# Kernel optimization log

Measured on AMD Instinct MI355X. Metric: run time of the kernel, lower is better.

Reference implementation:

```python
import jax, jax.numpy as jnp
import numpy as np

B, S, D, H, L = 4, 2048, 256, 4, 2
DK = D // H
V, T = 32000, 1000


def setup_inputs() -> dict:
    key = jax.random.key(0)
    ks = jax.random.split(key, 20)
    sc = 0.02
    event_emb = jax.random.normal(ks[0], (V, D), jnp.float32) * sc
    event_emb = event_emb.at[0].set(0.0)  # padding_idx=0
    time_emb = jax.random.normal(ks[1], (T, D), jnp.float32) * sc
    inp = {
        "x": jax.random.randint(ks[2], (B, S), 0, V, jnp.int32),
        "time_deltas": jax.random.randint(ks[3], (B, S), 0, T, jnp.int32),
        "mask": jax.random.randint(ks[4], (B, S), 0, 2, jnp.int32),
        "event_emb": event_emb,
        "time_emb": time_emb,
        "Wq": jax.random.normal(ks[5], (L, D, D), jnp.float32) * sc,
        "bq": jnp.zeros((L, D), jnp.float32),
        "Wk": jax.random.normal(ks[6], (L, D, D), jnp.float32) * sc,
        "bk": jnp.zeros((L, D), jnp.float32),
        "Wv": jax.random.normal(ks[7], (L, D, D), jnp.float32) * sc,
        "bv": jnp.zeros((L, D), jnp.float32),
        "time_proj": jax.random.normal(ks[8], (L, T, H), jnp.float32) * sc,
        "Wo": jax.random.normal(ks[9], (L, D, D), jnp.float32) * sc,
        "bo": jnp.zeros((L, D), jnp.float32),
        "ln_g": jnp.ones((L, D), jnp.float32),
        "ln_b": jnp.zeros((L, D), jnp.float32),
        "Wc1": jax.random.normal(ks[10], (D, D // 2), jnp.float32) * sc,
        "bc1": jnp.zeros((D // 2,), jnp.float32),
        "Wc2": jax.random.normal(ks[11], (D // 2, 1), jnp.float32) * sc,
        "bc2": jnp.zeros((1,), jnp.float32),
    }
    return inp


def _layernorm(h, g, b, eps=1e-5):
    mu = jnp.mean(h, -1, keepdims=True)
    var = jnp.mean(jnp.square(h - mu), -1, keepdims=True)
    return (h - mu) * jax.lax.rsqrt(var + eps) * g + b


def _attn(h, t_bins, mask, Wq, bq, Wk, bk, Wv, bv, tp, Wo, bo):
    b, s, d = h.shape
    q = (h @ Wq + bq).reshape(b, s, H, DK)
    k = (h @ Wk + bk).reshape(b, s, H, DK)
    v = (h @ Wv + bv).reshape(b, s, H, DK)
    scores = jnp.einsum("bqhd,bkhd->bhqk", q, k) / np.sqrt(DK).astype(np.float32)
    time_bias = tp[t_bins]  # [b,s,H] -> bias per key position
    scores = scores + jnp.transpose(time_bias, (0, 2, 1))[:, :, None, :]
    scores = jnp.where(mask[:, None, None, :] == 0, -1e9, scores)
    attn = jax.nn.softmax(scores, axis=-1)
    ctx = jnp.einsum("bhqk,bkhd->bqhd", attn, v).reshape(b, s, d)
    return ctx @ Wo + bo


def reference(x, time_deltas, mask, event_emb, time_emb, Wq, bq, Wk, bk, Wv, bv,
              time_proj, Wo, bo, ln_g, ln_b, Wc1, bc1, Wc2, bc2):
    t_bins = jnp.clip(time_deltas, 0, T - 1)
    h = event_emb[x] + time_emb[t_bins]
    for l in range(L):
        h = _attn(h, t_bins, mask, Wq[l], bq[l], Wk[l], bk[l], Wv[l], bv[l],
                  time_proj[l], Wo[l], bo[l])
        h = _layernorm(h, ln_g[l], ln_b[l])
    last = h[:, -1, :]
    hid = jax.nn.relu(last @ Wc1 + bc1)
    return jax.nn.sigmoid(hid @ Wc2 + bc2)
```

## Files before the change

kernel.cpp:

```cpp
#include <hip/hip_runtime.h>
#include <math.h>

namespace {

constexpr int NB = 4, NS = 2048, ND = 256, NH = 4, NDK = 64, NL = 2, NT = 1000;
constexpr float L2E = 1.44269504089f;
constexpr float QSCALE = 0.125f * L2E;

typedef short bfx8 __attribute__((ext_vector_type(8)));
typedef float f32x4 __attribute__((ext_vector_type(4)));
typedef float f32x16 __attribute__((ext_vector_type(16)));

static __device__ __forceinline__ short f2bf(float f) {
  union { float f; unsigned u; } v; v.f = f;
  unsigned u = v.u;
  unsigned r = (u + 0x7fffu + ((u >> 16) & 1u)) >> 16;
  return (short)r;
}
static __device__ __forceinline__ float bf2f(short s) {
  union { float f; unsigned u; } v; v.u = ((unsigned)(unsigned short)s) << 16;
  return v.f;
}
static __device__ __forceinline__ float exp2_hw(float x) {
  float r;
  asm("v_exp_f32 %0, %1" : "=v"(r) : "v"(x));
  return r;
}
static __device__ __forceinline__ unsigned cvt_pk_bf16(float lo, float hi) {
  unsigned d;
  asm("v_cvt_pk_bf16_f32 %0, %1, %2" : "=v"(d) : "v"(lo), "v"(hi));
  return d;
}

__global__ __launch_bounds__(256) void k_packem(const int* __restrict__ x,
                                                const int* __restrict__ td,
                                                const float* __restrict__ ee,
                                                const float* __restrict__ te,
                                                short* __restrict__ hb,
                                                const float* __restrict__ Wq,
                                                const float* __restrict__ Wk,
                                                const float* __restrict__ Wv,
                                                const float* __restrict__ Wo,
                                                const float* __restrict__ bq,
                                                const float* __restrict__ bk,
                                                const float* __restrict__ bv,
                                                short* __restrict__ wqkvT,
                                                short* __restrict__ woT,
                                                float* __restrict__ bqkv) {
  if (blockIdx.x < 128) {
    __shared__ float t[64][65];
    int bi = blockIdx.x;
    int z = bi >> 4, l = z >> 2, mat = z & 3;
    const float* src;
    short* dst;
    float scale = 1.f;
    if (mat == 0)      { src = Wq + (size_t)l * 65536; dst = wqkvT + (size_t)l * 768 * 256; scale = QSCALE; }
    else if (mat == 1) { src = Wk + (size_t)l * 65536; dst = wqkvT + (size_t)l * 768 * 256 + 256 * 256; }
    else if (mat == 2) { src = Wv + (size_t)l * 65536; dst = wqkvT + (size_t)l * 768 * 256 + 512 * 256; }
    else               { src = Wo + (size_t)l * 65536; dst = woT + (size_t)l * 65536; }
    int k0 = (bi & 3) * 64, n0 = ((bi >> 2) & 3) * 64;
    int c = threadIdx.x & 63, r4 = threadIdx.x >> 6;
    #pragma unroll
    for (int rr = 0; rr < 64; rr += 4) t[rr + r4][c] = src[(size_t)(k0 + rr + r4) * 256 + n0 + c];
    __syncthreads();
    #pragma unroll
    for (int rr = 0; rr < 64; rr += 4) {
      int n = rr + r4;
      dst[(size_t)(n0 + n) * 256 + k0 + c] = f2bf(t[c][n] * scale);
    }
    if (mat == 0 && (bi & 15) == 0) {
      for (int cc = threadIdx.x; cc < 768; cc += 256) {
        float v = cc < 256 ? bq[l * 256 + cc] * QSCALE
                           : (cc < 512 ? bk[l * 256 + cc - 256] : bv[l * 256 + cc - 512]);
        bqkv[l * 768 + cc] = v;
      }
    }
  } else {
    int lane = threadIdx.x & 63, r4 = threadIdx.x >> 6;
    int row = (blockIdx.x - 128) * 4 + r4;
    int xi = x[row];
    int tb = td[row];
    tb = tb < 0 ? 0 : (tb >= NT ? NT - 1 : tb);
    float4 e = ((const float4*)&ee[(size_t)xi * ND])[lane];
    float4 tv = ((const float4*)&te[(size_t)tb * ND])[lane];
    short4 ob;
    ob.x = f2bf(e.x + tv.x); ob.y = f2bf(e.y + tv.y);
    ob.z = f2bf(e.z + tv.z); ob.w = f2bf(e.w + tv.w);
    ((short4*)&hb[(size_t)row * ND])[lane] = ob;
  }
}

template <int OUT_BF16>
__global__ __launch_bounds__(256) void k_gemm(const short* __restrict__ A,
                                              const short* __restrict__ BT,
                                              const float* __restrict__ bias,
                                              void* __restrict__ C, int ldc,
                                              int mb_mul, int mb_add, int n_base) {
  constexpr int LP = 76;
  __shared__ short at[64][LP];
  __shared__ short bt[128][LP];
  int tid = threadIdx.x;
  int w = tid >> 6, lane = tid & 63, ln15 = lane & 15, g = lane >> 4;
  int m0 = (blockIdx.x * mb_mul + mb_add) * 64;
  int n0 = n_base + blockIdx.y * 128;
  int srow = tid >> 2, scol = (tid & 3) * 16;
  int brow = tid >> 1, bcol = (tid & 1) * 32;

  f32x4 acc[8];
  #pragma unroll
  for (int nt = 0; nt < 8; ++nt) acc[nt] = (f32x4){0.f, 0.f, 0.f, 0.f};

  bfx8 a0, a1, b0, b1, b2, b3;
  auto LOAD = [&](int kk0) {
    const short* as = &A[(size_t)(m0 + srow) * 256 + kk0 + scol];
    a0 = *(const bfx8*)as; a1 = *(const bfx8*)(as + 8);
    const short* bs = &BT[(size_t)(n0 + brow) * 256 + kk0 + bcol];
    b0 = *(const bfx8*)bs; b1 = *(const bfx8*)(bs + 8);
    b2 = *(const bfx8*)(bs + 16); b3 = *(const bfx8*)(bs + 24);
  };
  LOAD(0);
  for (int kk0 = 0; kk0 < 256; kk0 += 64) {
    __syncthreads();
    *(bfx8*)&at[srow][scol] = a0; *(bfx8*)&at[srow][scol + 8] = a1;
    *(bfx8*)&bt[brow][bcol] = b0; *(bfx8*)&bt[brow][bcol + 8] = b1;
    *(bfx8*)&bt[brow][bcol + 16] = b2; *(bfx8*)&bt[brow][bcol + 24] = b3;
    __syncthreads();
    if (kk0 + 64 < 256) LOAD(kk0 + 64);
    #pragma unroll
    for (int ks = 0; ks < 2; ++ks) {
      bfx8 af = *(const bfx8*)&at[w * 16 + ln15][ks * 32 + g * 8];
      #pragma unroll
      for (int nt = 0; nt < 8; ++nt) {
        bfx8 bf = *(const bfx8*)&bt[nt * 16 + ln15][ks * 32 + g * 8];
        acc[nt] = __builtin_amdgcn_mfma_f32_16x16x32_bf16(af, bf, acc[nt], 0, 0, 0);
      }
    }
  }

  #pragma unroll
  for (int nt = 0; nt < 8; ++nt) {
    int col = n0 + nt * 16 + ln15;
    float bb = bias[col];
    #pragma unroll
    for (int r = 0; r < 4; ++r) {
      int row = m0 + w * 16 + g * 4 + r;
      float val = acc[nt][r] + bb;
      if (OUT_BF16) ((short*)C)[(size_t)row * ldc + col] = f2bf(val);
      else          ((float*)C)[(size_t)row * ldc + col] = val;
    }
  }
}

__global__ __launch_bounds__(256) void k_pmerge(const short* __restrict__ partO,
                                                const float* __restrict__ partML,
                                                const short* __restrict__ BT,
                                                const float* __restrict__ bias,
                                                short* __restrict__ C) {
  constexpr int LP = 76;
  constexpr int NC = 2;
  __shared__ short at[64][LP];
  __shared__ short bt[128][LP];
  int tid = threadIdx.x;
  int w = tid >> 6, lane = tid & 63, ln15 = lane & 15, g = lane >> 4;
  int m0 = blockIdx.x * 64;
  int n0 = blockIdx.y * 128;
  int srow = tid >> 2, scol = (tid & 3) * 16;
  int brow = tid >> 1, bcol = (tid & 1) * 32;

  int grow = m0 + srow;
  int b = grow >> 11, s = grow & 2047;

  f32x4 acc[8];
  #pragma unroll
  for (int nt = 0; nt < 8; ++nt) acc[nt] = (f32x4){0.f, 0.f, 0.f, 0.f};

  bfx8 a0, a1, b0_, b1_, b2_, b3_;
  auto LOAD = [&](int kk0) {
    int hh2 = kk0 >> 6;
    size_t rbase = (size_t)(b * NH + hh2) * NS + s;
    float2 ml[NC];
    float M = -1e30f;
    #pragma unroll
    for (int c = 0; c < NC; ++c) {
      ml[c] = *(const float2*)&partML[(rbase + (size_t)c * 16 * NS) * 2];
      M = fmaxf(M, ml[c].x);
    }
    float wgt[NC], L = 0.f;
    #pragma unroll
    for (int c = 0; c < NC; ++c) { wgt[c] = exp2_hw(ml[c].x - M); L += ml[c].y * wgt[c]; }
    float inv = 1.f / L;
    float av[16];
    #pragma unroll
    for (int i = 0; i < 16; ++i) av[i] = 0.f;
    #pragma unroll
    for (int c = 0; c < NC; ++c) {
      float wc = wgt[c] * inv;
      size_t row = rbase + (size_t)c * 16 * NS;
      union { int4 v; short sh[8]; } ua, ub;
      ua.v = *(const int4*)&partO[row * 64 + scol];
      ub.v = *(const int4*)&partO[row * 64 + scol + 8];
      #pragma unroll
      for (int i = 0; i < 8; ++i) {
        av[i]     = fmaf(bf2f(ua.sh[i]), wc, av[i]);
        av[8 + i] = fmaf(bf2f(ub.sh[i]), wc, av[8 + i]);
      }
    }
    union { bfx8 v; short sh[8]; } pa, pb;
    #pragma unroll
    for (int i = 0; i < 8; ++i) { pa.sh[i] = f2bf(av[i]); pb.sh[i] = f2bf(av[8 + i]); }
    a0 = pa.v; a1 = pb.v;
    const short* bs = &BT[(size_t)(n0 + brow) * 256 + kk0 + bcol];
    b0_ = *(const bfx8*)bs; b1_ = *(const bfx8*)(bs + 8);
    b2_ = *(const bfx8*)(bs + 16); b3_ = *(const bfx8*)(bs + 24);
  };
  LOAD(0);
  for (int kk0 = 0; kk0 < 256; kk0 += 64) {
    __syncthreads();
    *(bfx8*)&at[srow][scol] = a0; *(bfx8*)&at[srow][scol + 8] = a1;
    *(bfx8*)&bt[brow][bcol] = b0_; *(bfx8*)&bt[brow][bcol + 8] = b1_;
    *(bfx8*)&bt[brow][bcol + 16] = b2_; *(bfx8*)&bt[brow][bcol + 24] = b3_;
    __syncthreads();
    if (kk0 + 64 < 256) LOAD(kk0 + 64);
    #pragma unroll
    for (int ks = 0; ks < 2; ++ks) {
      bfx8 af = *(const bfx8*)&at[w * 16 + ln15][ks * 32 + g * 8];
      #pragma unroll
      for (int nt = 0; nt < 8; ++nt) {
        bfx8 bf = *(const bfx8*)&bt[nt * 16 + ln15][ks * 32 + g * 8];
        acc[nt] = __builtin_amdgcn_mfma_f32_16x16x32_bf16(af, bf, acc[nt], 0, 0, 0);
      }
    }
  }

  #pragma unroll
  for (int nt = 0; nt < 8; ++nt) {
    int col = n0 + nt * 16 + ln15;
    float bb = bias[col];
    #pragma unroll
    for (int r = 0; r < 4; ++r) {
      int row = m0 + w * 16 + g * 4 + r;
      C[(size_t)row * 256 + col] = f2bf(acc[nt][r] + bb);
    }
  }
}

__global__ __launch_bounds__(256) void k_gmerge(const short* __restrict__ partO,
                                                const float* __restrict__ partML,
                                                const short* __restrict__ BT,
                                                const float* __restrict__ bias,
                                                float* __restrict__ C) {
  constexpr int LP = 76;
  constexpr int NC = 16;
  __shared__ short at[64][LP];
  __shared__ short bt[128][LP];
  int tid = threadIdx.x;
  int w = tid >> 6, lane = tid & 63, ln15 = lane & 15, g = lane >> 4;
  int m0 = (blockIdx.x * 32 + 31) * 64;
  int n0 = blockIdx.y * 128;
  int srow = tid >> 2, scol = (tid & 3) * 16;
  int brow = tid >> 1, bcol = (tid & 1) * 32;

  int grow = m0 + srow;
  int b = grow >> 11, s = grow & 2047;
  int qloc = s - (NS - 128);

  f32x4 acc[8];
  #pragma unroll
  for (int nt = 0; nt < 8; ++nt) acc[nt] = (f32x4){0.f, 0.f, 0.f, 0.f};

  bfx8 a0, a1, b0_, b1_, b2_, b3_;
  auto LOAD = [&](int kk0) {
    int hh2 = kk0 >> 6;
    size_t rbase = (size_t)(b * NH + hh2) * 128 + qloc;
    float M = -1e30f;
    float mls[NC], lls[NC];
    #pragma unroll
    for (int c = 0; c < NC; ++c) {
      float2 ml = *(const float2*)&partML[(rbase + (size_t)c * 16 * 128) * 2];
      mls[c] = ml.x; lls[c] = ml.y;
      M = fmaxf(M, ml.x);
    }
    float L = 0.f, wgt[NC];
    #pragma unroll
    for (int c = 0; c < NC; ++c) { wgt[c] = exp2_hw(mls[c] - M); L += lls[c] * wgt[c]; }
    float inv = 1.f / L;
    float av[16];
    #pragma unroll
    for (int i = 0; i < 16; ++i) av[i] = 0.f;
    #pragma unroll
    for (int c = 0; c < NC; ++c) {
      float wc = wgt[c] * inv;
      size_t row = rbase + (size_t)c * 16 * 128;
      union { int4 v; short sh[8]; } ua, ub;
      ua.v = *(const int4*)&partO[row * 64 + scol];
      ub.v = *(const int4*)&partO[row * 64 + scol + 8];
      #pragma unroll
      for (int i = 0; i < 8; ++i) {
        av[i]     = fmaf(bf2f(ua.sh[i]), wc, av[i]);
        av[8 + i] = fmaf(bf2f(ub.sh[i]), wc, av[8 + i]);
      }
    }
    union { bfx8 v; short sh[8]; } pa, pb;
    #pragma unroll
    for (int i = 0; i < 8; ++i) { pa.sh[i] = f2bf(av[i]); pb.sh[i] = f2bf(av[8 + i]); }
    a0 = pa.v; a1 = pb.v;
    const short* bs = &BT[(size_t)(n0 + brow) * 256 + kk0 + bcol];
    b0_ = *(const bfx8*)bs; b1_ = *(const bfx8*)(bs + 8);
    b2_ = *(const bfx8*)(bs + 16); b3_ = *(const bfx8*)(bs + 24);
  };
  LOAD(0);
  for (int kk0 = 0; kk0 < 256; kk0 += 64) {
    __syncthreads();
    *(bfx8*)&at[srow][scol] = a0; *(bfx8*)&at[srow][scol + 8] = a1;
    *(bfx8*)&bt[brow][bcol] = b0_; *(bfx8*)&bt[brow][bcol + 8] = b1_;
    *(bfx8*)&bt[brow][bcol + 16] = b2_; *(bfx8*)&bt[brow][bcol + 24] = b3_;
    __syncthreads();
    if (kk0 + 64 < 256) LOAD(kk0 + 64);
    #pragma unroll
    for (int ks = 0; ks < 2; ++ks) {
      bfx8 af = *(const bfx8*)&at[w * 16 + ln15][ks * 32 + g * 8];
      #pragma unroll
      for (int nt = 0; nt < 8; ++nt) {
        bfx8 bf = *(const bfx8*)&bt[nt * 16 + ln15][ks * 32 + g * 8];
        acc[nt] = __builtin_amdgcn_mfma_f32_16x16x32_bf16(af, bf, acc[nt], 0, 0, 0);
      }
    }
  }

  #pragma unroll
  for (int nt = 0; nt < 8; ++nt) {
    int col = n0 + nt * 16 + ln15;
    float bb = bias[col];
    #pragma unroll
    for (int r = 0; r < 4; ++r) {
      int row = m0 + w * 16 + g * 4 + r;
      C[(size_t)row * 256 + col] = acc[nt][r] + bb;
    }
  }
}

__global__ __launch_bounds__(256) void k_frag(const short* __restrict__ qkv,
                                              const int* __restrict__ td,
                                              const int* __restrict__ mask,
                                              const float* __restrict__ tp,
                                              short* __restrict__ vT,
                                              float* __restrict__ sbias_g) {
  __shared__ short vl[64][72];
  int tile = blockIdx.x, hh = blockIdx.y, b = blockIdx.z;
  int t = threadIdx.x;
  int k0 = tile * 64;
  {
    int key = t >> 2, dg = (t & 3) * 16;
    const short* vsrc = &qkv[(size_t)(b * NS + k0 + key) * 768 + 512 + hh * NDK + dg];
    bfx8 v0 = *(const bfx8*)vsrc, v1 = *(const bfx8*)(vsrc + 8);
    *(bfx8*)&vl[key][dg] = v0;
    *(bfx8*)&vl[key][dg + 8] = v1;
  }
  if (t < 64) {
    int kk = k0 + t;
    int tb = td[b * NS + kk];
    tb = tb < 0 ? 0 : (tb >= NT ? NT - 1 : tb);
    sbias_g[(size_t)(b * NH + hh) * NS + kk] = mask[b * NS + kk] ? tp[tb * NH + hh] * L2E : -1e9f;
  }
  __syncthreads();
  int dim = t >> 2, c0 = (t & 3) * 16;
  short outv[16];
  #pragma unroll
  for (int j = 0; j < 16; ++j) outv[j] = vl[c0 + j][dim];
  short* dst = &vT[(((size_t)(b * NH + hh) * 32 + tile) * 64 + dim) * 64 + c0];
  *(int4*)dst = *(const int4*)outv;
  *(int4*)(dst + 8) = *(const int4*)(outv + 8);
}

__global__ __launch_bounds__(256) void k_attn(const short* __restrict__ qkv,
                                              const short* __restrict__ vT,
                                              const float* __restrict__ sbias_g,
                                              short* __restrict__ partO,
                                              float* __restrict__ partML,
                                              int q_base, int qcount, int nchunk) {
  constexpr int LP = 76;
  __shared__ short kt[64][LP];
  __shared__ short vt[64][LP];
  __shared__ float sbias[64];

  int tid = threadIdx.x;
  int w = tid >> 6, lane = tid & 63, q31 = lane & 31, hl = lane >> 5;
  int b = blockIdx.z, hh = blockIdx.y;
  int bh = b * NH + hh;
  int qtile = blockIdx.x / nchunk;
  int chunk = blockIdx.x - qtile * nchunk;
  int niter = NS / (64 * nchunk);
  int tbase = chunk * niter;
  int q0 = q_base + qtile * 128;
  int qq = q0 + w * 32 + q31;

  bfx8 aq[4];
  #pragma unroll
  for (int ki = 0; ki < 4; ++ki)
    aq[ki] = *(const bfx8*)&qkv[(size_t)(b * NS + qq) * 768 + hh * NDK + ki * 16 + hl * 8];

  f32x16 o[2];
  #pragma unroll
  for (int dt = 0; dt < 2; ++dt)
    #pragma unroll
    for (int i = 0; i < 16; ++i) o[dt][i] = 0.f;
  float m = -1e30f, lsum = 0.f;

  int srow = tid >> 2, scg = (tid & 3) * 16;

  bfx8 kr0, kr1, vr0, vr1;
  float br = 0.f;
  auto loadset = [&](int it) {
    int tt = tbase + it;
    int k0 = tt * 64;
    const short* ksrc = &qkv[(size_t)(b * NS + k0 + srow) * 768 + 256 + hh * NDK + scg];
    kr0 = *(const bfx8*)ksrc; kr1 = *(const bfx8*)(ksrc + 8);
    const short* vsrc = &vT[(((size_t)bh * 32 + tt) * 64 + srow) * 64 + scg];
    vr0 = *(const bfx8*)vsrc; vr1 = *(const bfx8*)(vsrc + 8);
    if (tid < 64) br = sbias_g[(size_t)bh * NS + k0 + tid];
  };

  loadset(0);
  for (int it = 0; it < niter; ++it) {
    __syncthreads();
    *(bfx8*)&kt[srow][scg] = kr0;
    *(bfx8*)&kt[srow][scg + 8] = kr1;
    *(bfx8*)&vt[srow][scg] = vr0;
    *(bfx8*)&vt[srow][scg + 8] = vr1;
    if (tid < 64) sbias[tid] = br;
    __syncthreads();
    if (it + 1 < niter) loadset(it + 1);

    f32x16 c[2];
    #pragma unroll
    for (int kt2 = 0; kt2 < 2; ++kt2)
      #pragma unroll
      for (int i = 0; i < 16; ++i) c[kt2][i] = 0.f;
    __builtin_amdgcn_s_setprio(1);
    #pragma unroll
    for (int kt2 = 0; kt2 < 2; ++kt2) {
      #pragma unroll
      for (int ki = 0; ki < 4; ++ki) {
        bfx8 kf = *(const bfx8*)&kt[kt2 * 32 + q31][ki * 16 + hl * 8];
        c[kt2] = __builtin_amdgcn_mfma_f32_32x32x16_bf16(kf, aq[ki], c[kt2], 0, 0, 0);
      }
    }
    __builtin_amdgcn_s_setprio(0);

    #pragma unroll
    for (int kt2 = 0; kt2 < 2; ++kt2) {
      #pragma unroll
      for (int rg = 0; rg < 4; ++rg) {
        float4 bb = *(const float4*)&sbias[kt2 * 32 + rg * 8 + hl * 4];
        c[kt2][rg * 4 + 0] += bb.x; c[kt2][rg * 4 + 1] += bb.y;
        c[kt2][rg * 4 + 2] += bb.z; c[kt2][rg * 4 + 3] += bb.w;
      }
    }
    float rm = c[0][0];
    #pragma unroll
    for (int kt2 = 0; kt2 < 2; ++kt2)
      #pragma unroll
      for (int i = 0; i < 16; ++i) rm = fmaxf(rm, c[kt2][i]);
    rm = fmaxf(rm, __shfl_xor(rm, 32, 64));
    if (__any(rm > m + 10.f)) {
      float nm = fmaxf(m, rm);
      float scl = exp2_hw(m - nm);
      m = nm;
      lsum *= scl;
      #pragma unroll
      for (int dt = 0; dt < 2; ++dt)
        #pragma unroll
        for (int i = 0; i < 16; ++i) o[dt][i] *= scl;
    }
    float ts = 0.f;
    #pragma unroll
    for (int kt2 = 0; kt2 < 2; ++kt2)
      #pragma unroll
      for (int i = 0; i < 16; ++i) { c[kt2][i] = exp2_hw(c[kt2][i] - m); ts += c[kt2][i]; }
    lsum += ts;

    __builtin_amdgcn_s_setprio(1);
    #pragma unroll
    for (int kt2 = 0; kt2 < 2; ++kt2) {
      #pragma unroll
      for (int ks = 0; ks < 2; ++ks) {
        unsigned pa0 = cvt_pk_bf16(c[kt2][8 * ks + 0], c[kt2][8 * ks + 1]);
        unsigned pa1 = cvt_pk_bf16(c[kt2][8 * ks + 2], c[kt2][8 * ks + 3]);
        unsigned pb0 = cvt_pk_bf16(c[kt2][8 * ks + 4], c[kt2][8 * ks + 5]);
        unsigned pb1 = cvt_pk_bf16(c[kt2][8 * ks + 6], c[kt2][8 * ks + 7]);
        asm volatile("v_permlane32_swap_b32 %0, %1" : "+v"(pa0), "+v"(pb0));
        asm volatile("v_permlane32_swap_b32 %0, %1" : "+v"(pa1), "+v"(pb1));
        union { unsigned u[4]; bfx8 v; } pf;
        pf.u[0] = pa0; pf.u[1] = pa1; pf.u[2] = pb0; pf.u[3] = pb1;
        #pragma unroll
        for (int dt = 0; dt < 2; ++dt) {
          bfx8 vf = *(const bfx8*)&vt[dt * 32 + q31][kt2 * 32 + ks * 16 + hl * 8];
          o[dt] = __builtin_amdgcn_mfma_f32_32x32x16_bf16(vf, pf.v, o[dt], 0, 0, 0);
        }
      }
    }
    __builtin_amdgcn_s_setprio(0);
  }

  lsum += __shfl_xor(lsum, 32, 64);

  size_t rowi = (size_t)(chunk * 16 + bh) * qcount + qtile * 128 + w * 32 + q31;
  #pragma unroll
  for (int dt = 0; dt < 2; ++dt) {
    #pragma unroll
    for (int rg = 0; rg < 4; ++rg) {
      int2 pk;
      pk.x = (int)cvt_pk_bf16(o[dt][rg * 4 + 0], o[dt][rg * 4 + 1]);
      pk.y = (int)cvt_pk_bf16(o[dt][rg * 4 + 2], o[dt][rg * 4 + 3]);
      *(int2*)&partO[rowi * 64 + dt * 32 + rg * 8 + hl * 4] = pk;
    }
  }
  if (hl == 0) { partML[rowi * 2] = m; partML[rowi * 2 + 1] = lsum; }
}

__global__ __launch_bounds__(256) void k_lnb(const short* __restrict__ in,
                                             short* __restrict__ hb,
                                             const float* __restrict__ g_,
                                             const float* __restrict__ b_) {
  int lane = threadIdx.x & 63, r4 = threadIdx.x >> 6;
  size_t row = (size_t)blockIdx.y * NS + blockIdx.x * 4 + r4;
  short4 sv = ((const short4*)&in[row * ND])[lane];
  float vx = bf2f(sv.x), vy = bf2f(sv.y), vz = bf2f(sv.z), vw = bf2f(sv.w);
  float s = vx + vy + vz + vw;
  #pragma unroll
  for (int off = 1; off < 64; off <<= 1) s += __shfl_xor(s, off, 64);
  float mu = s * (1.f / ND);
  float dx = vx - mu, dy = vy - mu, dz = vz - mu, dw = vw - mu;
  float q = dx * dx + dy * dy + dz * dz + dw * dw;
  #pragma unroll
  for (int off = 1; off < 64; off <<= 1) q += __shfl_xor(q, off, 64);
  float rr = rsqrtf(q * (1.f / ND) + 1e-5f);
  float4 gg = ((const float4*)g_)[lane];
  float4 bb = ((const float4*)b_)[lane];
  short4 ob;
  ob.x = f2bf(dx * rr * gg.x + bb.x);
  ob.y = f2bf(dy * rr * gg.y + bb.y);
  ob.z = f2bf(dz * rr * gg.z + bb.z);
  ob.w = f2bf(dw * rr * gg.w + bb.w);
  ((short4*)&hb[row * ND])[lane] = ob;
}

__global__ __launch_bounds__(256) void k_lnhead(const float* __restrict__ h,
                                                const float* __restrict__ g_,
                                                const float* __restrict__ b_,
                                                const float* __restrict__ Wc1,
                                                const float* __restrict__ bc1,
                                                const float* __restrict__ Wc2,
                                                const float* __restrict__ bc2,
                                                float* __restrict__ out) {
  __shared__ float rowv[256];
  __shared__ float red[256];
  int b = blockIdx.x, j = threadIdx.x;
  float v = h[(size_t)(b * NS + NS - 1) * ND + j];
  red[j] = v;
  __syncthreads();
  for (int off = 128; off > 0; off >>= 1) {
    if (j < off) red[j] += red[j + off];
    __syncthreads();
  }
  float mu = red[0] * (1.f / ND);
  __syncthreads();
  float d = v - mu;
  red[j] = d * d;
  __syncthreads();
  for (int off = 128; off > 0; off >>= 1) {
    if (j < off) red[j] += red[j + off];
    __syncthreads();
  }
  float rr = rsqrtf(red[0] * (1.f / ND) + 1e-5f);
  rowv[j] = d * rr * g_[j] + b_[j];
  __syncthreads();
  float hid = 0.f;
  if (j < 128) {
    hid = bc1[j];
    for (int dd = 0; dd < ND; ++dd) hid = fmaf(rowv[dd], Wc1[dd * 128 + j], hid);
    hid = fmaxf(hid, 0.f) * Wc2[j];
  }
  __syncthreads();
  red[j] = j < 128 ? hid : 0.f;
  __syncthreads();
  for (int off = 64; off > 0; off >>= 1) {
    if (j < off) red[j] += red[j + off];
    __syncthreads();
  }
  if (j == 0) out[b] = 1.f / (1.f + __expf(-(red[0] + bc2[0])));
}

}

extern "C" void kernel_launch(void* const* d_in, const int* in_sizes, int n_in,
                              void* d_out, int out_size, void* d_ws, size_t ws_size,
                              hipStream_t stream) {
  const int* x = (const int*)d_in[0];
  const int* td = (const int*)d_in[1];
  const int* mask = (const int*)d_in[2];
  const float* ee = (const float*)d_in[3];
  const float* te = (const float*)d_in[4];
  const float* Wq = (const float*)d_in[5];
  const float* bq = (const float*)d_in[6];
  const float* Wk = (const float*)d_in[7];
  const float* bk = (const float*)d_in[8];
  const float* Wv = (const float*)d_in[9];
  const float* bv = (const float*)d_in[10];
  const float* tp = (const float*)d_in[11];
  const float* Wo = (const float*)d_in[12];
  const float* bo = (const float*)d_in[13];
  const float* lng = (const float*)d_in[14];
  const float* lnb = (const float*)d_in[15];
  const float* Wc1 = (const float*)d_in[16];
  const float* bc1 = (const float*)d_in[17];
  const float* Wc2 = (const float*)d_in[18];
  const float* bc2 = (const float*)d_in[19];
  float* out = (float*)d_out;

  char* ws = (char*)d_ws;
  const size_t M = (size_t)NB * NS;
  short* qkv     = (short*)(ws);
  float* h       = (float*)(ws + (12 << 20));
  short* hb      = (short*)(ws + (20 << 20));
  short* vT      = (short*)(ws + (24 << 20));
  float* sbias_g = (float*)(ws + (28 << 20));
  short* wqkvT   = (short*)(ws + (28 << 20) + (128 << 10));
  short* woT     = (short*)(ws + (28 << 20) + (896 << 10));
  float* bqkv    = (float*)(ws + (28 << 20) + (1152 << 10));
  short* partO   = (short*)(ws + (30 << 20));
  float* partML  = (float*)(ws + (47 << 20));
  short* hraw    = (short*)(ws + (48 << 20));

  k_packem<<<128 + NB * NS / 4, 256, 0, stream>>>(x, td, ee, te, hb,
                                                  Wq, Wk, Wv, Wo, bq, bk, bv,
                                                  wqkvT, woT, bqkv);

  for (int l = 0; l < NL; ++l) {
    const short* wqkvTl = wqkvT + (size_t)l * 768 * 256;
    const short* woTl = woT + (size_t)l * 65536;
    const float* bqkvl = bqkv + (size_t)l * 768;
    const float* bol = bo + (size_t)l * ND;
    const float* tpl = tp + (size_t)l * NT * NH;
    const float* lngl = lng + (size_t)l * ND;
    const float* lnbl = lnb + (size_t)l * ND;
    const bool last = (l == NL - 1);

    if (!last) {
      k_gemm<1><<<dim3(M / 64, 6), 256, 0, stream>>>(hb, wqkvTl, bqkvl, qkv, 768, 1, 0, 0);
    } else {
      k_gemm<1><<<dim3(M / 64, 4), 256, 0, stream>>>(hb, wqkvTl, bqkvl, qkv, 768, 1, 0, 256);
      k_gemm<1><<<dim3(NB, 2), 256, 0, stream>>>(hb, wqkvTl, bqkvl, qkv, 768, 32, 31, 0);
    }

    k_frag<<<dim3(32, NH, NB), 256, 0, stream>>>(qkv, td, mask, tpl, vT, sbias_g);

    if (!last) {
      k_attn<<<dim3(16 * 2, NH, NB), 256, 0, stream>>>(qkv, vT, sbias_g,
                                                       partO, partML, 0, NS, 2);
      k_pmerge<<<dim3(M / 64, 2), 256, 0, stream>>>(partO, partML, woTl, bol, hraw);
      k_lnb<<<dim3(NS / 4, NB), 256, 0, stream>>>(hraw, hb, lngl, lnbl);
    } else {
      k_attn<<<dim3(16, NH, NB), 256, 0, stream>>>(qkv, vT, sbias_g,
                                                   partO, partML, NS - 128, 128, 16);
      k_gmerge<<<dim3(NB, 2), 256, 0, stream>>>(partO, partML, woTl, bol, h);
      k_lnhead<<<NB, 256, 0, stream>>>(h, lngl, lnbl, Wc1, bc1, Wc2, bc2, out);
    }
  }
}
```

Before: 117.3 us.

## Fuse V transpose into V projection GEMM and precompute score bias upfront

Removes the k_frag kernel. A new GEMM variant computes the V projection and writes its output directly in the transposed per-tile vT layout that attention consumes, so V is no longer written to qkv and then re-read for transposition. The per-key time/mask score bias for both layers is now computed once inside the initial packing kernel. This saves one launch per layer and the V round-trip through memory, at the cost of an extra GEMM launch and narrower short4 scattered stores for vT.

Measured after the change: 119.2 us. Within noise of the previous version (+1.6%).

```diff
diff --git a/kernel.cpp b/kernel.cpp
--- a/kernel.cpp
+++ b/kernel.cpp
@@ -34,6 +34,8 @@
 
 __global__ __launch_bounds__(256) void k_packem(const int* __restrict__ x,
                                                 const int* __restrict__ td,
+                                                const int* __restrict__ mask,
+                                                const float* __restrict__ tp,
                                                 const float* __restrict__ ee,
                                                 const float* __restrict__ te,
                                                 short* __restrict__ hb,
@@ -46,7 +48,8 @@
                                                 const float* __restrict__ bv,
                                                 short* __restrict__ wqkvT,
                                                 short* __restrict__ woT,
-                                                float* __restrict__ bqkv) {
+                                                float* __restrict__ bqkv,
+                                                float* __restrict__ sbias_g) {
   if (blockIdx.x < 128) {
     __shared__ float t[64][65];
     int bi = blockIdx.x;
@@ -75,7 +78,7 @@
         bqkv[l * 768 + cc] = v;
       }
     }
-  } else {
+  } else if (blockIdx.x < 128 + 2048) {
     int lane = threadIdx.x & 63, r4 = threadIdx.x >> 6;
     int row = (blockIdx.x - 128) * 4 + r4;
     int xi = x[row];
@@ -87,6 +90,16 @@
     ob.x = f2bf(e.x + tv.x); ob.y = f2bf(e.y + tv.y);
     ob.z = f2bf(e.z + tv.z); ob.w = f2bf(e.w + tv.w);
     ((short4*)&hb[(size_t)row * ND])[lane] = ob;
+  } else {
+    int flat = (blockIdx.x - 2176) * 256 + threadIdx.x;
+    int l = flat >> 15;
+    int rem = flat & 32767;
+    int bh = rem >> 11, key = rem & 2047;
+    int b = bh >> 2, hh = bh & 3;
+    int tb = td[b * NS + key];
+    tb = tb < 0 ? 0 : (tb >= NT ? NT - 1 : tb);
+    float v = mask[b * NS + key] ? tp[(size_t)l * NT * NH + tb * NH + hh] * L2E : -1e9f;
+    sbias_g[(size_t)(l * 16 + bh) * NS + key] = v;
   }
 }
 
@@ -151,6 +164,68 @@
   }
 }
 
+__global__ __launch_bounds__(256) void k_gemmv(const short* __restrict__ A,
+                                               const short* __restrict__ BT,
+                                               const float* __restrict__ bias,
+                                               short* __restrict__ vT,
+                                               int mb_mul, int mb_add) {
+  constexpr int LP = 76;
+  __shared__ short at[64][LP];
+  __shared__ short bt[128][LP];
+  int tid = threadIdx.x;
+  int w = tid >> 6, lane = tid & 63, ln15 = lane & 15, g = lane >> 4;
+  int m0 = (blockIdx.x * mb_mul + mb_add) * 64;
+  int n0 = blockIdx.y * 128;
+  int srow = tid >> 2, scol = (tid & 3) * 16;
+  int brow = tid >> 1, bcol = (tid & 1) * 32;
+
+  f32x4 acc[8];
+  #pragma unroll
+  for (int nt = 0; nt < 8; ++nt) acc[nt] = (f32x4){0.f, 0.f, 0.f, 0.f};
+
+  bfx8 a0, a1, b0, b1, b2, b3;
+  auto LOAD = [&](int kk0) {
+    const short* as = &A[(size_t)(m0 + srow) * 256 + kk0 + scol];
+    a0 = *(const bfx8*)as; a1 = *(const bfx8*)(as + 8);
+    const short* bs = &BT[(size_t)(n0 + brow) * 256 + kk0 + bcol];
+    b0 = *(const bfx8*)bs; b1 = *(const bfx8*)(bs + 8);
+    b2 = *(const bfx8*)(bs + 16); b3 = *(const bfx8*)(bs + 24);
+  };
+  LOAD(0);
+  for (int kk0 = 0; kk0 < 256; kk0 += 64) {
+    __syncthreads();
+    *(bfx8*)&at[srow][scol] = a0; *(bfx8*)&at[srow][scol + 8] = a1;
+    *(bfx8*)&bt[brow][bcol] = b0; *(bfx8*)&bt[brow][bcol + 8] = b1;
+    *(bfx8*)&bt[brow][bcol + 16] = b2; *(bfx8*)&bt[brow][bcol + 24] = b3;
+    __syncthreads();
+    if (kk0 + 64 < 256) LOAD(kk0 + 64);
+    #pragma unroll
+    for (int ks = 0; ks < 2; ++ks) {
+      bfx8 af = *(const bfx8*)&at[w * 16 + ln15][ks * 32 + g * 8];
+      #pragma unroll
+      for (int nt = 0; nt < 8; ++nt) {
+        bfx8 bf = *(const bfx8*)&bt[nt * 16 + ln15][ks * 32 + g * 8];
+        acc[nt] = __builtin_amdgcn_mfma_f32_16x16x32_bf16(af, bf, acc[nt], 0, 0, 0);
+      }
+    }
+  }
+
+  int b = m0 >> 11, s0 = m0 & 2047;
+  int tile = s0 >> 6, key0 = w * 16 + g * 4;
+  #pragma unroll
+  for (int nt = 0; nt < 8; ++nt) {
+    int col = n0 + nt * 16 + ln15;
+    int hh = col >> 6, dim = col & 63;
+    float bb = bias[col];
+    short4 ov;
+    ov.x = f2bf(acc[nt][0] + bb);
+    ov.y = f2bf(acc[nt][1] + bb);
+    ov.z = f2bf(acc[nt][2] + bb);
+    ov.w = f2bf(acc[nt][3] + bb);
+    *(short4*)&vT[(((size_t)(b * NH + hh) * 32 + tile) * 64 + dim) * 64 + key0] = ov;
+  }
+}
+
 __global__ __launch_bounds__(256) void k_pmerge(const short* __restrict__ partO,
                                                 const float* __restrict__ partML,
                                                 const short* __restrict__ BT,
@@ -337,39 +412,6 @@
       C[(size_t)row * 256 + col] = acc[nt][r] + bb;
     }
   }
-}
-
-__global__ __launch_bounds__(256) void k_frag(const short* __restrict__ qkv,
-                                              const int* __restrict__ td,
-                                              const int* __restrict__ mask,
-                                              const float* __restrict__ tp,
-                                              short* __restrict__ vT,
-                                              float* __restrict__ sbias_g) {
-  __shared__ short vl[64][72];
-  int tile = blockIdx.x, hh = blockIdx.y, b = blockIdx.z;
-  int t = threadIdx.x;
-  int k0 = tile * 64;
-  {
-    int key = t >> 2, dg = (t & 3) * 16;
-    const short* vsrc = &qkv[(size_t)(b * NS + k0 + key) * 768 + 512 + hh * NDK + dg];
-    bfx8 v0 = *(const bfx8*)vsrc, v1 = *(const bfx8*)(vsrc + 8);
-    *(bfx8*)&vl[key][dg] = v0;
-    *(bfx8*)&vl[key][dg + 8] = v1;
-  }
-  if (t < 64) {
-    int kk = k0 + t;
-    int tb = td[b * NS + kk];
-    tb = tb < 0 ? 0 : (tb >= NT ? NT - 1 : tb);
-    sbias_g[(size_t)(b * NH + hh) * NS + kk] = mask[b * NS + kk] ? tp[tb * NH + hh] * L2E : -1e9f;
-  }
-  __syncthreads();
-  int dim = t >> 2, c0 = (t & 3) * 16;
-  short outv[16];
-  #pragma unroll
-  for (int j = 0; j < 16; ++j) outv[j] = vl[c0 + j][dim];
-  short* dst = &vT[(((size_t)(b * NH + hh) * 32 + tile) * 64 + dim) * 64 + c0];
-  *(int4*)dst = *(const int4*)outv;
-  *(int4*)(dst + 8) = *(const int4*)(outv + 8);
 }
 
 __global__ __launch_bounds__(256) void k_attn(const short* __restrict__ qkv,
@@ -624,44 +666,42 @@
   float* h       = (float*)(ws + (12 << 20));
   short* hb      = (short*)(ws + (20 << 20));
   short* vT      = (short*)(ws + (24 << 20));
-  float* sbias_g = (float*)(ws + (28 << 20));
   short* wqkvT   = (short*)(ws + (28 << 20) + (128 << 10));
   short* woT     = (short*)(ws + (28 << 20) + (896 << 10));
   float* bqkv    = (float*)(ws + (28 << 20) + (1152 << 10));
   short* partO   = (short*)(ws + (30 << 20));
   float* partML  = (float*)(ws + (47 << 20));
   short* hraw    = (short*)(ws + (48 << 20));
-
-  k_packem<<<128 + NB * NS / 4, 256, 0, stream>>>(x, td, ee, te, hb,
-                                                  Wq, Wk, Wv, Wo, bq, bk, bv,
-                                                  wqkvT, woT, bqkv);
+  float* sbias_g = (float*)(ws + (52 << 20));
+
+  k_packem<<<128 + NB * NS / 4 + 256, 256, 0, stream>>>(x, td, mask, tp, ee, te, hb,
+                                                        Wq, Wk, Wv, Wo, bq, bk, bv,
+                                                        wqkvT, woT, bqkv, sbias_g);
 
   for (int l = 0; l < NL; ++l) {
     const short* wqkvTl = wqkvT + (size_t)l * 768 * 256;
+    const short* wvTl = wqkvTl + 512 * 256;
     const short* woTl = woT + (size_t)l * 65536;
     const float* bqkvl = bqkv + (size_t)l * 768;
+    const float* bvl = bqkvl + 512;
     const float* bol = bo + (size_t)l * ND;
-    const float* tpl = tp + (size_t)l * NT * NH;
     const float* lngl = lng + (size_t)l * ND;
     const float* lnbl = lnb + (size_t)l * ND;
+    const float* sbl = sbias_g + (size_t)l * 16 * NS;
     const bool last = (l == NL - 1);
 
     if (!last) {
-      k_gemm<1><<<dim3(M / 64, 6), 256, 0, stream>>>(hb, wqkvTl, bqkvl, qkv, 768, 1, 0, 0);
-    } else {
-      k_gemm<1><<<dim3(M / 64, 4), 256, 0, stream>>>(hb, wqkvTl, bqkvl, qkv, 768, 1, 0, 256);
-      k_gemm<1><<<dim3(NB, 2), 256, 0, stream>>>(hb, wqkvTl, bqkvl, qkv, 768, 32, 31, 0);
-    }
-
-    k_frag<<<dim3(32, NH, NB), 256, 0, stream>>>(qkv, td, mask, tpl, vT, sbias_g);
-
-    if (!last) {
-      k_attn<<<dim3(16 * 2, NH, NB), 256, 0, stream>>>(qkv, vT, sbias_g,
+      k_gemm<1><<<dim3(M / 64, 4), 256, 0, stream>>>(hb, wqkvTl, bqkvl, qkv, 768, 1, 0, 0);
+      k_gemmv<<<dim3(M / 64, 2), 256, 0, stream>>>(hb, wvTl, bvl, vT, 1, 0);
+      k_attn<<<dim3(16 * 2, NH, NB), 256, 0, stream>>>(qkv, vT, sbl,
                                                        partO, partML, 0, NS, 2);
       k_pmerge<<<dim3(M / 64, 2), 256, 0, stream>>>(partO, partML, woTl, bol, hraw);
       k_lnb<<<dim3(NS / 4, NB), 256, 0, stream>>>(hraw, hb, lngl, lnbl);
     } else {
-      k_attn<<<dim3(16, NH, NB), 256, 0, stream>>>(qkv, vT, sbias_g,
+      k_gemm<1><<<dim3(M / 64, 2), 256, 0, stream>>>(hb, wqkvTl, bqkvl, qkv, 768, 1, 0, 256);
+      k_gemmv<<<dim3(M / 64, 2), 256, 0, stream>>>(hb, wvTl, bvl, vT, 1, 0);
+      k_gemm<1><<<dim3(NB, 2), 256, 0, stream>>>(hb, wqkvTl, bqkvl, qkv, 768, 32, 31, 0);
+      k_attn<<<dim3(16, NH, NB), 256, 0, stream>>>(qkv, vT, sbl,
                                                    partO, partML, NS - 128, 128, 16);
       k_gmerge<<<dim3(NB, 2), 256, 0, stream>>>(partO, partML, woTl, bol, h);
       k_lnhead<<<NB, 256, 0, stream>>>(h, lngl, lnbl, Wc1, bc1, Wc2, bc2, out);
```
